# Optimization experiments

Hardware: AMD Instinct MI355X
Metric: run time of the kernel (lower is better)

## Reference

```python
import jax, jax.numpy as jnp
import numpy as np

N_NODES = 100000
N_EDGES = 800000
FEAT = 128
HID = 128
NUM_CLASSES = 2
NUM_GRAPHS = 64


def setup_inputs() -> dict:
    key = jax.random.key(0)
    ks = jax.random.split(key, 20)
    s_feat = 1.0 / np.sqrt(FEAT)
    s_hid = 1.0 / np.sqrt(HID)
    s_h2 = 1.0 / np.sqrt(HID // 2)
    inp = {
        "x": jax.random.normal(ks[0], (N_NODES, FEAT), jnp.float32),
        "edge_index": jax.random.randint(ks[1], (2, N_EDGES), 0, N_NODES, jnp.int32),
        "batch": jnp.sort(jax.random.randint(ks[2], (N_NODES,), 0, NUM_GRAPHS, jnp.int32)),
        "fc1_w": jax.random.uniform(ks[3], (FEAT, HID), jnp.float32, -s_feat, s_feat),
        "fc1_b": jax.random.uniform(ks[4], (HID,), jnp.float32, -s_feat, s_feat),
        "conv1_rel_w": jax.random.uniform(ks[5], (HID, HID), jnp.float32, -s_hid, s_hid),
        "conv1_rel_b": jax.random.uniform(ks[6], (HID,), jnp.float32, -s_hid, s_hid),
        "conv1_root_w": jax.random.uniform(ks[7], (HID, HID), jnp.float32, -s_hid, s_hid),
        "fc2_w": jax.random.uniform(ks[8], (HID, HID), jnp.float32, -s_hid, s_hid),
        "fc2_b": jax.random.uniform(ks[9], (HID,), jnp.float32, -s_hid, s_hid),
        "conv2_rel_w": jax.random.uniform(ks[10], (HID, HID), jnp.float32, -s_hid, s_hid),
        "conv2_rel_b": jax.random.uniform(ks[11], (HID,), jnp.float32, -s_hid, s_hid),
        "conv2_root_w": jax.random.uniform(ks[12], (HID, HID), jnp.float32, -s_hid, s_hid),
        "fc3_w": jax.random.uniform(ks[13], (HID, HID), jnp.float32, -s_hid, s_hid),
        "fc3_b": jax.random.uniform(ks[14], (HID,), jnp.float32, -s_hid, s_hid),
        "fc4_w": jax.random.uniform(ks[15], (HID, HID // 2), jnp.float32, -s_hid, s_hid),
        "fc4_b": jax.random.uniform(ks[16], (HID // 2,), jnp.float32, -s_hid, s_hid),
        "fc5_w": jax.random.uniform(ks[17], (HID // 2, NUM_CLASSES), jnp.float32, -s_h2, s_h2),
        "fc5_b": jax.random.uniform(ks[18], (NUM_CLASSES,), jnp.float32, -s_h2, s_h2),
    }
    return inp


def reference(x, edge_index, batch,
              fc1_w, fc1_b, conv1_rel_w, conv1_rel_b, conv1_root_w,
              fc2_w, fc2_b, conv2_rel_w, conv2_rel_b, conv2_root_w,
              fc3_w, fc3_b, fc4_w, fc4_b, fc5_w, fc5_b):
    lrelu = lambda z: jax.nn.leaky_relu(z, 0.01)
    src, dst = edge_index[0], edge_index[1]

    def graph_conv(h, rel_w, rel_b, root_w):
        # PyG GraphConv (aggr='add'): sum_{j in N(i)} x_j @ W_rel + b + x_i @ W_root
        msg = h[src]                                               # [E, H] gather
        agg = jax.ops.segment_sum(msg, dst, num_segments=h.shape[0])  # [N, H] scatter-add
        return agg @ rel_w + rel_b + h @ root_w

    h = lrelu(x @ fc1_w + fc1_b)
    h = lrelu(graph_conv(h, conv1_rel_w, conv1_rel_b, conv1_root_w))
    h = lrelu(h @ fc2_w + fc2_b)
    h = lrelu(graph_conv(h, conv2_rel_w, conv2_rel_b, conv2_root_w))

    # global mean pool over graph ids
    sums = jax.ops.segment_sum(h, batch, num_segments=NUM_GRAPHS)              # [G, H]
    cnts = jax.ops.segment_sum(jnp.ones((h.shape[0], 1), h.dtype), batch,
                               num_segments=NUM_GRAPHS)                        # [G, 1]
    g = sums / jnp.maximum(cnts, 1.0)

    g = lrelu(g @ fc3_w + fc3_b)
    g = lrelu(g @ fc4_w + fc4_b)
    return g @ fc5_w + fc5_b
```

## Files before the change

kernel.cpp:

```cpp
#include <hip/hip_runtime.h>
#include <hip/hip_bf16.h>

#define NN 100000
#define NE 800000
#define PCH 16
#define MAXDEG 40

typedef __attribute__((ext_vector_type(8))) short bf16x8;
typedef __attribute__((ext_vector_type(4))) float f32x4;

__device__ __forceinline__ unsigned short f2b(float f){
  unsigned int u = __float_as_uint(f);
  unsigned int r = (u + 0x7FFFu + ((u>>16)&1u)) >> 16;
  return (unsigned short)r;
}
__device__ __forceinline__ float b2f(unsigned int s){
  return __uint_as_float(s<<16);
}
__device__ __forceinline__ float lrelu(float v){ return v > 0.f ? v : 0.01f*v; }

struct WPtrs { const float* src[6]; unsigned short* dst[6]; };
__global__ void wcvt_kernel(WPtrs p){
  int wi = blockIdx.y;
  int idx = blockIdx.x*256 + threadIdx.x;
  int n = idx >> 7, k = idx & 127;
  p.dst[wi][idx] = f2b(p.src[wi][k*128 + n]);
  (void)n;
}

__global__ __launch_bounds__(256) void fc1_fill_kernel(
    const float* __restrict__ x, const unsigned short* __restrict__ W0t,
    const float* __restrict__ bias, unsigned short* __restrict__ outb, int M,
    const int* __restrict__ ei, int* __restrict__ cnt, int* __restrict__ slot, int E)
{
  __shared__ unsigned short sA[128*72];
  __shared__ unsigned short sW[128*72];
  const int bi = blockIdx.x;
  const int role = bi % 3;
  if (role != 0){
    int fi = (bi/3)*2 + (role-1);
    int base = (fi*256 + threadIdx.x)*2;
    if (base + 2 <= E){
      int2 d2 = *(const int2*)&ei[E + base];
      int2 s2 = *(const int2*)&ei[base];
      int p0 = atomicAdd(&cnt[d2.x], 1);
      int p1 = atomicAdd(&cnt[d2.y], 1);
      if (p0 < MAXDEG) slot[d2.x*MAXDEG + p0] = s2.x;
      if (p1 < MAXDEG) slot[d2.y*MAXDEG + p1] = s2.y;
    }
    return;
  }
  const int tid = threadIdx.x;
  const int w = tid >> 6, l = tid & 63;
  const int row0 = (bi/3) * 128;

  f32x4 acc[2][8];
  #pragma unroll
  for (int r=0;r<2;++r)
    #pragma unroll
    for (int n=0;n<8;++n) acc[r][n] = (f32x4){0.f,0.f,0.f,0.f};

  for (int p=0; p<2; ++p){
    const int koff = p * 64;
    __syncthreads();
    #pragma unroll
    for (int it=0; it<4; ++it){
      int idx = it*256 + tid;
      int r = idx >> 3, c = (idx & 7) * 8;
      int grow = row0 + r;
      bf16x8 v;
      if (grow < M){
        float4 f0 = *(const float4*)(x + grow*128 + koff + c);
        float4 f1 = *(const float4*)(x + grow*128 + koff + c + 4);
        v[0]=(short)f2b(f0.x); v[1]=(short)f2b(f0.y); v[2]=(short)f2b(f0.z); v[3]=(short)f2b(f0.w);
        v[4]=(short)f2b(f1.x); v[5]=(short)f2b(f1.y); v[6]=(short)f2b(f1.z); v[7]=(short)f2b(f1.w);
      } else {
        #pragma unroll
        for (int j=0;j<8;++j) v[j]=0;
      }
      *(bf16x8*)&sA[r*72 + c] = v;
    }
    #pragma unroll
    for (int it=0; it<4; ++it){
      int idx = it*256 + tid;
      int r = idx >> 3, c = (idx & 7) * 8;
      *(bf16x8*)&sW[r*72 + c] = *(const bf16x8*)(W0t + r*128 + koff + c);
    }
    __syncthreads();

    #pragma unroll
    for (int kc=0; kc<2; ++kc){
      const int kb = kc*32 + ((l>>4)<<3);
      bf16x8 a0 = *(const bf16x8*)&sA[(w*32 +      (l&15))*72 + kb];
      bf16x8 a1 = *(const bf16x8*)&sA[(w*32 + 16 + (l&15))*72 + kb];
      #pragma unroll
      for (int nf=0; nf<8; ++nf){
        bf16x8 b = *(const bf16x8*)&sW[(nf*16 + (l&15))*72 + kb];
        acc[0][nf] = __builtin_amdgcn_mfma_f32_16x16x32_bf16(a0, b, acc[0][nf], 0, 0, 0);
        acc[1][nf] = __builtin_amdgcn_mfma_f32_16x16x32_bf16(a1, b, acc[1][nf], 0, 0, 0);
      }
    }
  }

  #pragma unroll
  for (int r=0;r<2;++r){
    int rb = row0 + w*32 + r*16 + ((l>>4)<<2);
    #pragma unroll
    for (int nf=0;nf<8;++nf){
      int col = nf*16 + (l&15);
      float bv = bias[col];
      #pragma unroll
      for (int q=0;q<4;++q){
        int rr = rb + q;
        if (rr < M){
          outb[rr*128 + col] = f2b(lrelu(acc[r][nf][q] + bv));
        }
      }
    }
  }
}

__global__ __launch_bounds__(256) void agg_kernel(
    const unsigned short* __restrict__ h, const int* __restrict__ cnt,
    const int* __restrict__ slot, unsigned short* __restrict__ agg, int N){
  int node = (blockIdx.x*4 + threadIdx.y)*2 + (threadIdx.x >> 5);
  if (node >= N) return;
  int hl = threadIdx.x & 31;
  int deg = min(cnt[node], MAXDEG);
  const int* sl = slot + node*MAXDEG;
  float a0=0.f, a1=0.f, a2=0.f, a3=0.f;
  int j = 0;
  for (; j + 8 <= deg; j += 8){
    int4 ia = *(const int4*)&sl[j];
    int4 ib = *(const int4*)&sl[j+4];
    uint2 v0 = *(const uint2*)&h[ia.x*128 + hl*4];
    uint2 v1 = *(const uint2*)&h[ia.y*128 + hl*4];
    uint2 v2 = *(const uint2*)&h[ia.z*128 + hl*4];
    uint2 v3 = *(const uint2*)&h[ia.w*128 + hl*4];
    uint2 v4 = *(const uint2*)&h[ib.x*128 + hl*4];
    uint2 v5 = *(const uint2*)&h[ib.y*128 + hl*4];
    uint2 v6 = *(const uint2*)&h[ib.z*128 + hl*4];
    uint2 v7 = *(const uint2*)&h[ib.w*128 + hl*4];
    a0 += b2f(v0.x&0xffff)+b2f(v1.x&0xffff)+b2f(v2.x&0xffff)+b2f(v3.x&0xffff)
        + b2f(v4.x&0xffff)+b2f(v5.x&0xffff)+b2f(v6.x&0xffff)+b2f(v7.x&0xffff);
    a1 += b2f(v0.x>>16)+b2f(v1.x>>16)+b2f(v2.x>>16)+b2f(v3.x>>16)
        + b2f(v4.x>>16)+b2f(v5.x>>16)+b2f(v6.x>>16)+b2f(v7.x>>16);
    a2 += b2f(v0.y&0xffff)+b2f(v1.y&0xffff)+b2f(v2.y&0xffff)+b2f(v3.y&0xffff)
        + b2f(v4.y&0xffff)+b2f(v5.y&0xffff)+b2f(v6.y&0xffff)+b2f(v7.y&0xffff);
    a3 += b2f(v0.y>>16)+b2f(v1.y>>16)+b2f(v2.y>>16)+b2f(v3.y>>16)
        + b2f(v4.y>>16)+b2f(v5.y>>16)+b2f(v6.y>>16)+b2f(v7.y>>16);
  }
  for (; j + 4 <= deg; j += 4){
    int4 ia = *(const int4*)&sl[j];
    uint2 v0 = *(const uint2*)&h[ia.x*128 + hl*4];
    uint2 v1 = *(const uint2*)&h[ia.y*128 + hl*4];
    uint2 v2 = *(const uint2*)&h[ia.z*128 + hl*4];
    uint2 v3 = *(const uint2*)&h[ia.w*128 + hl*4];
    a0 += b2f(v0.x&0xffff)+b2f(v1.x&0xffff)+b2f(v2.x&0xffff)+b2f(v3.x&0xffff);
    a1 += b2f(v0.x>>16)+b2f(v1.x>>16)+b2f(v2.x>>16)+b2f(v3.x>>16);
    a2 += b2f(v0.y&0xffff)+b2f(v1.y&0xffff)+b2f(v2.y&0xffff)+b2f(v3.y&0xffff);
    a3 += b2f(v0.y>>16)+b2f(v1.y>>16)+b2f(v2.y>>16)+b2f(v3.y>>16);
  }
  for (; j < deg; ++j){
    int s = sl[j];
    uint2 v = *(const uint2*)&h[s*128 + hl*4];
    a0 += b2f(v.x&0xffff); a1 += b2f(v.x>>16);
    a2 += b2f(v.y&0xffff); a3 += b2f(v.y>>16);
  }
  uint2 o;
  o.x = ((unsigned int)f2b(a1) << 16) | f2b(a0);
  o.y = ((unsigned int)f2b(a3) << 16) | f2b(a2);
  *(uint2*)&agg[node*128 + hl*4] = o;
}

__global__ __launch_bounds__(256) void convfc_kernel(
    const unsigned short* __restrict__ A0, const unsigned short* __restrict__ A1,
    const unsigned short* __restrict__ W0t, const unsigned short* __restrict__ W1t,
    const float* __restrict__ bias1,
    const unsigned short* __restrict__ W2t, const float* __restrict__ bias2,
    unsigned short* __restrict__ outb, int M)
{
  __shared__ unsigned short sA[128*72];
  __shared__ unsigned short sW[128*72];
  const int tid = threadIdx.x;
  const int w = tid >> 6, l = tid & 63;
  const int row0 = blockIdx.x * 128;

  f32x4 acc[2][8];
  #pragma unroll
  for (int r=0;r<2;++r)
    #pragma unroll
    for (int n=0;n<8;++n) acc[r][n] = (f32x4){0.f,0.f,0.f,0.f};

  for (int p=0; p<4; ++p){
    const int ai = p >> 1;
    const int koff = (p & 1) * 64;
    const unsigned short* Ag = ai ? A1 : A0;
    const unsigned short* Wt = ai ? W1t : W0t;
    __syncthreads();
    #pragma unroll
    for (int it=0; it<4; ++it){
      int idx = it*256 + tid;
      int r = idx >> 3, c = (idx & 7) * 8;
      int grow = row0 + r;
      bf16x8 v;
      if (grow < M){
        v = *(const bf16x8*)(Ag + grow*128 + koff + c);
      } else {
        #pragma unroll
        for (int j=0;j<8;++j) v[j]=0;
      }
      *(bf16x8*)&sA[r*72 + c] = v;
    }
    #pragma unroll
    for (int it=0; it<4; ++it){
      int idx = it*256 + tid;
      int r = idx >> 3, c = (idx & 7) * 8;
      *(bf16x8*)&sW[r*72 + c] = *(const bf16x8*)(Wt + r*128 + koff + c);
    }
    __syncthreads();
    #pragma unroll
    for (int kc=0; kc<2; ++kc){
      const int kb = kc*32 + ((l>>4)<<3);
      bf16x8 a0 = *(const bf16x8*)&sA[(w*32 +      (l&15))*72 + kb];
      bf16x8 a1 = *(const bf16x8*)&sA[(w*32 + 16 + (l&15))*72 + kb];
      #pragma unroll
      for (int nf=0; nf<8; ++nf){
        bf16x8 b = *(const bf16x8*)&sW[(nf*16 + (l&15))*72 + kb];
        acc[0][nf] = __builtin_amdgcn_mfma_f32_16x16x32_bf16(a0, b, acc[0][nf], 0, 0, 0);
        acc[1][nf] = __builtin_amdgcn_mfma_f32_16x16x32_bf16(a1, b, acc[1][nf], 0, 0, 0);
      }
    }
  }

  unsigned short v16[2][8][4];
  #pragma unroll
  for (int r=0;r<2;++r)
    #pragma unroll
    for (int nf=0;nf<8;++nf){
      float bv = bias1[nf*16 + (l&15)];
      #pragma unroll
      for (int q=0;q<4;++q) v16[r][nf][q] = f2b(lrelu(acc[r][nf][q] + bv));
    }

  f32x4 acc2[2][8];
  #pragma unroll
  for (int r=0;r<2;++r)
    #pragma unroll
    for (int n=0;n<8;++n) acc2[r][n] = (f32x4){0.f,0.f,0.f,0.f};

  for (int ph=0; ph<2; ++ph){
    __syncthreads();
    #pragma unroll
    for (int r=0;r<2;++r)
      #pragma unroll
      for (int nfl=0;nfl<4;++nfl){
        int nf = ph*4 + nfl;
        int cl = nfl*16 + (l&15);
        #pragma unroll
        for (int q=0;q<4;++q){
          int row = w*32 + r*16 + ((l>>4)<<2) + q;
          sA[row*72 + cl] = v16[r][nf][q];
        }
      }
    #pragma unroll
    for (int it=0; it<4; ++it){
      int idx = it*256 + tid;
      int r = idx >> 3, c = (idx & 7) * 8;
      *(bf16x8*)&sW[r*72 + c] = *(const bf16x8*)(W2t + r*128 + ph*64 + c);
    }
    __syncthreads();
    #pragma unroll
    for (int kc=0; kc<2; ++kc){
      const int kb = kc*32 + ((l>>4)<<3);
      bf16x8 a0 = *(const bf16x8*)&sA[(w*32 +      (l&15))*72 + kb];
      bf16x8 a1 = *(const bf16x8*)&sA[(w*32 + 16 + (l&15))*72 + kb];
      #pragma unroll
      for (int nf=0; nf<8; ++nf){
        bf16x8 b = *(const bf16x8*)&sW[(nf*16 + (l&15))*72 + kb];
        acc2[0][nf] = __builtin_amdgcn_mfma_f32_16x16x32_bf16(a0, b, acc2[0][nf], 0, 0, 0);
        acc2[1][nf] = __builtin_amdgcn_mfma_f32_16x16x32_bf16(a1, b, acc2[1][nf], 0, 0, 0);
      }
    }
  }

  #pragma unroll
  for (int r=0;r<2;++r){
    int rb = row0 + w*32 + r*16 + ((l>>4)<<2);
    #pragma unroll
    for (int nf=0;nf<8;++nf){
      int col = nf*16 + (l&15);
      float bv = bias2[col];
      #pragma unroll
      for (int q=0;q<4;++q){
        int rr = rb + q;
        if (rr < M){
          outb[rr*128 + col] = f2b(lrelu(acc2[r][nf][q] + bv));
        }
      }
    }
  }
}

__global__ __launch_bounds__(256) void gemm2_kernel(
    const unsigned short* __restrict__ A0, const unsigned short* __restrict__ A1,
    const unsigned short* __restrict__ W0t, const unsigned short* __restrict__ W1t,
    const float* __restrict__ bias, unsigned short* __restrict__ outb, int M)
{
  __shared__ unsigned short sA[128*72];
  __shared__ unsigned short sW[128*72];
  const int tid = threadIdx.x;
  const int w = tid >> 6, l = tid & 63;
  const int row0 = blockIdx.x * 128;

  f32x4 acc[2][8];
  #pragma unroll
  for (int r=0;r<2;++r)
    #pragma unroll
    for (int n=0;n<8;++n) acc[r][n] = (f32x4){0.f,0.f,0.f,0.f};

  for (int p=0; p<4; ++p){
    const int ai = p >> 1;
    const int koff = (p & 1) * 64;
    const unsigned short* Ag = ai ? A1 : A0;
    const unsigned short* Wt = ai ? W1t : W0t;

    __syncthreads();
    #pragma unroll
    for (int it=0; it<4; ++it){
      int idx = it*256 + tid;
      int r = idx >> 3, c = (idx & 7) * 8;
      int grow = row0 + r;
      bf16x8 v;
      if (grow < M){
        v = *(const bf16x8*)(Ag + grow*128 + koff + c);
      } else {
        #pragma unroll
        for (int j=0;j<8;++j) v[j]=0;
      }
      *(bf16x8*)&sA[r*72 + c] = v;
    }
    #pragma unroll
    for (int it=0; it<4; ++it){
      int idx = it*256 + tid;
      int r = idx >> 3, c = (idx & 7) * 8;
      *(bf16x8*)&sW[r*72 + c] = *(const bf16x8*)(Wt + r*128 + koff + c);
    }
    __syncthreads();

    #pragma unroll
    for (int kc=0; kc<2; ++kc){
      const int kb = kc*32 + ((l>>4)<<3);
      bf16x8 a0 = *(const bf16x8*)&sA[(w*32 +      (l&15))*72 + kb];
      bf16x8 a1 = *(const bf16x8*)&sA[(w*32 + 16 + (l&15))*72 + kb];
      #pragma unroll
      for (int nf=0; nf<8; ++nf){
        bf16x8 b = *(const bf16x8*)&sW[(nf*16 + (l&15))*72 + kb];
        acc[0][nf] = __builtin_amdgcn_mfma_f32_16x16x32_bf16(a0, b, acc[0][nf], 0, 0, 0);
        acc[1][nf] = __builtin_amdgcn_mfma_f32_16x16x32_bf16(a1, b, acc[1][nf], 0, 0, 0);
      }
    }
  }

  #pragma unroll
  for (int r=0;r<2;++r){
    int rb = row0 + w*32 + r*16 + ((l>>4)<<2);
    #pragma unroll
    for (int nf=0;nf<8;++nf){
      int col = nf*16 + (l&15);
      float bv = bias[col];
      #pragma unroll
      for (int q=0;q<4;++q){
        int rr = rb + q;
        if (rr < M){
          outb[rr*128 + col] = f2b(lrelu(acc[r][nf][q] + bv));
        }
      }
    }
  }
}

__global__ void gbounds_kernel(const int* __restrict__ batch, int* __restrict__ gstart, int N){
  int g = threadIdx.x;
  if (g > 64) return;
  int lo = 0, hi = N;
  while (lo < hi){ int mid = (lo+hi)>>1; if (batch[mid] < g) lo = mid+1; else hi = mid; }
  gstart[g] = lo;
}

__global__ __launch_bounds__(256) void pool_kernel(
    const unsigned short* __restrict__ h, const int* __restrict__ gstart,
    float* __restrict__ gsum){
  int g = blockIdx.y;
  int s = gstart[g], e = gstart[g+1];
  int cnt = e - s;
  if (cnt <= 0) return;
  int len = (cnt + PCH - 1) / PCH;
  int r0 = s + blockIdx.x * len;
  int r1 = min(r0 + len, e);
  int w = threadIdx.x >> 6, l = threadIdx.x & 63;
  float ax = 0.f, ay = 0.f;
  for (int n = r0 + w; n < r1; n += 4){
    unsigned int v = *(const unsigned int*)&h[n*128 + l*2];
    ax += b2f(v & 0xffff);
    ay += b2f(v >> 16);
  }
  __shared__ float sm[4][128];
  sm[w][l*2]   = ax;
  sm[w][l*2+1] = ay;
  __syncthreads();
  int t = threadIdx.x;
  if (t < 128){
    float v = sm[0][t] + sm[1][t] + sm[2][t] + sm[3][t];
    atomicAdd(&gsum[g*128 + t], v);
  }
}

__global__ void head3_kernel(const float* gsum, const int* gstart, const float* w, const float* b, float* g3){
  int g = blockIdx.x, c = threadIdx.x;
  int cnt = gstart[g+1] - gstart[g];
  float inv = 1.f / (float)max(cnt, 1);
  float s = b[c];
  for (int k=0;k<128;++k) s += gsum[g*128+k]*inv * w[k*128 + c];
  g3[g*128 + c] = lrelu(s);
}
__global__ void head4_kernel(const float* g3, const float* w, const float* b, float* g4){
  int g = blockIdx.x, c = threadIdx.x;
  float s = b[c];
  for (int k=0;k<128;++k) s += g3[g*128+k] * w[k*64 + c];
  g4[g*64 + c] = lrelu(s);
}
__global__ void head5_kernel(const float* g4, const float* w, const float* b, float* out){
  int o = threadIdx.x;
  if (o < 128){
    int g = o >> 1, c = o & 1;
    float s = b[c];
    for (int k=0;k<64;++k) s += g4[g*64+k] * w[k*2 + c];
    out[o] = s;
  }
}

extern "C" void kernel_launch(void* const* d_in, const int* in_sizes, int n_in,
                              void* d_out, int out_size, void* d_ws, size_t ws_size,
                              hipStream_t stream){
  const float* x        = (const float*)d_in[0];
  const int*   ei       = (const int*)d_in[1];
  const int*   batch    = (const int*)d_in[2];
  const float* fc1_w    = (const float*)d_in[3];
  const float* fc1_b    = (const float*)d_in[4];
  const float* c1_rel_w = (const float*)d_in[5];
  const float* c1_rel_b = (const float*)d_in[6];
  const float* c1_root_w= (const float*)d_in[7];
  const float* fc2_w    = (const float*)d_in[8];
  const float* fc2_b    = (const float*)d_in[9];
  const float* c2_rel_w = (const float*)d_in[10];
  const float* c2_rel_b = (const float*)d_in[11];
  const float* c2_root_w= (const float*)d_in[12];
  const float* fc3_w    = (const float*)d_in[13];
  const float* fc3_b    = (const float*)d_in[14];
  const float* fc4_w    = (const float*)d_in[15];
  const float* fc4_b    = (const float*)d_in[16];
  const float* fc5_w    = (const float*)d_in[17];
  const float* fc5_b    = (const float*)d_in[18];

  char* ws = (char*)d_ws;
  size_t off = 0;
  auto alloc = [&](size_t bytes)->void*{
    void* p = ws + off;
    off = (off + bytes + 255) & ~(size_t)255;
    return p;
  };
  float* gsum   = (float*)alloc(64*128*4);
  int*   cnt    = (int*)  alloc((size_t)NN*4);
  size_t zero_bytes = off;
  int*   gstart = (int*)  alloc(65*4);
  int*   slot   = (int*)  alloc((size_t)NN*MAXDEG*4);
  unsigned short* Wt[6];
  for (int i=0;i<6;++i) Wt[i] = (unsigned short*)alloc(128*128*2);
  unsigned short* B1 = (unsigned short*)alloc((size_t)NN*128*2);
  unsigned short* B2 = (unsigned short*)alloc((size_t)NN*128*2);
  unsigned short* B3 = (unsigned short*)alloc((size_t)NN*128*2);
  float* g3 = (float*)alloc(64*128*4);
  float* g4 = (float*)alloc(64*64*4);
  (void)ws_size; (void)in_sizes; (void)n_in; (void)out_size;

  hipMemsetAsync(d_ws, 0, zero_bytes, stream);

  WPtrs wp;
  wp.src[0]=fc1_w;    wp.dst[0]=Wt[0];
  wp.src[1]=c1_rel_w; wp.dst[1]=Wt[1];
  wp.src[2]=c1_root_w;wp.dst[2]=Wt[2];
  wp.src[3]=fc2_w;    wp.dst[3]=Wt[3];
  wp.src[4]=c2_rel_w; wp.dst[4]=Wt[4];
  wp.src[5]=c2_root_w;wp.dst[5]=Wt[5];
  wcvt_kernel<<<dim3(64,6), 256, 0, stream>>>(wp);
  gbounds_kernel<<<1, 128, 0, stream>>>(batch, gstart, NN);

  const int GB   = (NN + 127)/128;
  const int AB   = (NN + 7)/8;
  const int FATB = 3*GB;

  fc1_fill_kernel<<<FATB, 256, 0, stream>>>(x, Wt[0], fc1_b, B1, NN, ei, cnt, slot, NE);
  agg_kernel<<<AB, dim3(64,4), 0, stream>>>(B1, cnt, slot, B3, NN);
  convfc_kernel<<<GB, 256, 0, stream>>>(B3, B1, Wt[1], Wt[2], c1_rel_b, Wt[3], fc2_b, B2, NN);
  agg_kernel<<<AB, dim3(64,4), 0, stream>>>(B2, cnt, slot, B3, NN);
  gemm2_kernel<<<GB, 256, 0, stream>>>(B3, B2, Wt[4], Wt[5], c2_rel_b, B1, NN);
  pool_kernel<<<dim3(PCH, 64), 256, 0, stream>>>(B1, gstart, gsum);
  head3_kernel<<<64, 128, 0, stream>>>(gsum, gstart, fc3_w, fc3_b, g3);
  head4_kernel<<<64, 64, 0, stream>>>(g3, fc4_w, fc4_b, g4);
  head5_kernel<<<1, 128, 0, stream>>>(g4, fc5_w, fc5_b, (float*)d_out);
}
```

Measured before the change: 256.3 us.

## Prefetch all A tiles into registers upfront and fold gbounds into wcvt kernel

In the convfc and gemm2 kernels, all four K-phase slices of the activation tile are loaded from global memory into registers before the MFMA loop. Each phase then only stores them to shared memory, so global load latency is exposed once rather than serialized per phase. This adds 16 bf16x8 registers per thread and may lower occupancy. Separately, the graph-bounds binary search is merged into the weight-conversion kernel as an extra grid row, removing one kernel launch.

```diff
diff --git a/kernel.cpp b/kernel.cpp
--- a/kernel.cpp
+++ b/kernel.cpp
@@ -20,12 +20,21 @@
 __device__ __forceinline__ float lrelu(float v){ return v > 0.f ? v : 0.01f*v; }
 
 struct WPtrs { const float* src[6]; unsigned short* dst[6]; };
-__global__ void wcvt_kernel(WPtrs p){
+__global__ void wcvt_kernel(WPtrs p, const int* __restrict__ batch, int* __restrict__ gstart, int N){
   int wi = blockIdx.y;
+  if (wi == 6){
+    if (blockIdx.x == 0){
+      int g = threadIdx.x;
+      if (g <= 64){
+        int lo = 0, hi = N;
+        while (lo < hi){ int mid = (lo+hi)>>1; if (batch[mid] < g) lo = mid+1; else hi = mid; }
+        gstart[g] = lo;
+      }
+    }
+    return;
+  }
   int idx = blockIdx.x*256 + threadIdx.x;
-  int n = idx >> 7, k = idx & 127;
-  p.dst[wi][idx] = f2b(p.src[wi][k*128 + n]);
-  (void)n;
+  p.dst[wi][idx] = f2b(p.src[wi][(idx & 127)*128 + (idx >> 7)]);
 }
 
 __global__ __launch_bounds__(256) void fc1_fill_kernel(
@@ -186,36 +195,41 @@
   const int w = tid >> 6, l = tid & 63;
   const int row0 = blockIdx.x * 128;
 
-  f32x4 acc[2][8];
-  #pragma unroll
-  for (int r=0;r<2;++r)
-    #pragma unroll
-    for (int n=0;n<8;++n) acc[r][n] = (f32x4){0.f,0.f,0.f,0.f};
-
+  bf16x8 pa[4][4];
+  #pragma unroll
   for (int p=0; p<4; ++p){
-    const int ai = p >> 1;
-    const int koff = (p & 1) * 64;
-    const unsigned short* Ag = ai ? A1 : A0;
-    const unsigned short* Wt = ai ? W1t : W0t;
-    __syncthreads();
+    const unsigned short* Ag = (p>>1) ? A1 : A0;
+    const int koff = (p&1)*64;
     #pragma unroll
     for (int it=0; it<4; ++it){
       int idx = it*256 + tid;
       int r = idx >> 3, c = (idx & 7) * 8;
       int grow = row0 + r;
-      bf16x8 v;
       if (grow < M){
-        v = *(const bf16x8*)(Ag + grow*128 + koff + c);
+        pa[p][it] = *(const bf16x8*)(Ag + grow*128 + koff + c);
       } else {
         #pragma unroll
-        for (int j=0;j<8;++j) v[j]=0;
-      }
-      *(bf16x8*)&sA[r*72 + c] = v;
-    }
-    #pragma unroll
-    for (int it=0; it<4; ++it){
-      int idx = it*256 + tid;
-      int r = idx >> 3, c = (idx & 7) * 8;
+        for (int j=0;j<8;++j) pa[p][it][j] = 0;
+      }
+    }
+  }
+
+  f32x4 acc[2][8];
+  #pragma unroll
+  for (int r=0;r<2;++r)
+    #pragma unroll
+    for (int n=0;n<8;++n) acc[r][n] = (f32x4){0.f,0.f,0.f,0.f};
+
+  #pragma unroll
+  for (int p=0; p<4; ++p){
+    const unsigned short* Wt = (p>>1) ? W1t : W0t;
+    const int koff = (p&1)*64;
+    __syncthreads();
+    #pragma unroll
+    for (int it=0; it<4; ++it){
+      int idx = it*256 + tid;
+      int r = idx >> 3, c = (idx & 7) * 8;
+      *(bf16x8*)&sA[r*72 + c] = pa[p][it];
       *(bf16x8*)&sW[r*72 + c] = *(const bf16x8*)(Wt + r*128 + koff + c);
     }
     __syncthreads();
@@ -249,6 +263,7 @@
     #pragma unroll
     for (int n=0;n<8;++n) acc2[r][n] = (f32x4){0.f,0.f,0.f,0.f};
 
+  #pragma unroll
   for (int ph=0; ph<2; ++ph){
     __syncthreads();
     #pragma unroll
@@ -313,37 +328,42 @@
   const int w = tid >> 6, l = tid & 63;
   const int row0 = blockIdx.x * 128;
 
-  f32x4 acc[2][8];
-  #pragma unroll
-  for (int r=0;r<2;++r)
-    #pragma unroll
-    for (int n=0;n<8;++n) acc[r][n] = (f32x4){0.f,0.f,0.f,0.f};
-
+  bf16x8 pa[4][4];
+  #pragma unroll
   for (int p=0; p<4; ++p){
-    const int ai = p >> 1;
-    const int koff = (p & 1) * 64;
-    const unsigned short* Ag = ai ? A1 : A0;
-    const unsigned short* Wt = ai ? W1t : W0t;
-
-    __syncthreads();
+    const unsigned short* Ag = (p>>1) ? A1 : A0;
+    const int koff = (p&1)*64;
     #pragma unroll
     for (int it=0; it<4; ++it){
       int idx = it*256 + tid;
       int r = idx >> 3, c = (idx & 7) * 8;
       int grow = row0 + r;
-      bf16x8 v;
       if (grow < M){
-        v = *(const bf16x8*)(Ag + grow*128 + koff + c);
+        pa[p][it] = *(const bf16x8*)(Ag + grow*128 + koff + c);
       } else {
         #pragma unroll
-        for (int j=0;j<8;++j) v[j]=0;
-      }
-      *(bf16x8*)&sA[r*72 + c] = v;
-    }
-    #pragma unroll
-    for (int it=0; it<4; ++it){
-      int idx = it*256 + tid;
-      int r = idx >> 3, c = (idx & 7) * 8;
+        for (int j=0;j<8;++j) pa[p][it][j] = 0;
+      }
+    }
+  }
+
+  f32x4 acc[2][8];
+  #pragma unroll
+  for (int r=0;r<2;++r)
+    #pragma unroll
+    for (int n=0;n<8;++n) acc[r][n] = (f32x4){0.f,0.f,0.f,0.f};
+
+  #pragma unroll
+  for (int p=0; p<4; ++p){
+    const unsigned short* Wt = (p>>1) ? W1t : W0t;
+    const int koff = (p&1)*64;
+
+    __syncthreads();
+    #pragma unroll
+    for (int it=0; it<4; ++it){
+      int idx = it*256 + tid;
+      int r = idx >> 3, c = (idx & 7) * 8;
+      *(bf16x8*)&sA[r*72 + c] = pa[p][it];
       *(bf16x8*)&sW[r*72 + c] = *(const bf16x8*)(Wt + r*128 + koff + c);
     }
     __syncthreads();
@@ -378,14 +398,6 @@
       }
     }
   }
-}
-
-__global__ void gbounds_kernel(const int* __restrict__ batch, int* __restrict__ gstart, int N){
-  int g = threadIdx.x;
-  if (g > 64) return;
-  int lo = 0, hi = N;
-  while (lo < hi){ int mid = (lo+hi)>>1; if (batch[mid] < g) lo = mid+1; else hi = mid; }
-  gstart[g] = lo;
 }
 
 __global__ __launch_bounds__(256) void pool_kernel(
@@ -493,8 +505,7 @@
   wp.src[3]=fc2_w;    wp.dst[3]=Wt[3];
   wp.src[4]=c2_rel_w; wp.dst[4]=Wt[4];
   wp.src[5]=c2_root_w;wp.dst[5]=Wt[5];
-  wcvt_kernel<<<dim3(64,6), 256, 0, stream>>>(wp);
-  gbounds_kernel<<<1, 128, 0, stream>>>(batch, gstart, NN);
+  wcvt_kernel<<<dim3(64,7), 256, 0, stream>>>(wp, batch, gstart, NN);
 
   const int GB   = (NN + 127)/128;
   const int AB   = (NN + 7)/8;
```

Result: faster. 244.6 us (-4.6%).
